# Optimization experiments

Hardware: AMD Instinct MI355X
Metric: run time of the kernel (lower is better)

## Reference

```python
import jax, jax.numpy as jnp
import numpy as np
from jax.ops import segment_sum

N0 = 50000
N1 = 50000
E = 300000
D = 128
L = 3
EPS_GIN = 0.1
COEF = 0.1
BN_EPS = 1e-5


def setup_inputs() -> dict:
    key = jax.random.key(0)
    ks = jax.random.split(key, 32)
    inp = {}
    inp['x0'] = jax.random.randint(ks[0], (N0, 2), 0, 3)
    inp['x1'] = jax.random.randint(ks[1], (N1, 2), 0, 3)
    inp['ei101'] = jax.random.randint(ks[2], (2, E), 0, N1)
    inp['ea101'] = jax.random.randint(ks[3], (E, 2), 0, 3)
    inp['ei110'] = jax.random.randint(ks[4], (2, E), 0, N0)  # src '1' -> dst '0' (N1==N0)
    inp['ea110'] = jax.random.randint(ks[5], (E, 2), 0, 3)
    inp['ei021'] = jax.random.randint(ks[6], (2, E), 0, N1)  # src '0' -> dst '1'
    inp['ea021'] = jax.random.randint(ks[7], (E, 2), 0, 3)
    inp['ei030'] = jax.random.randint(ks[8], (2, E), 0, N0)
    inp['ea030'] = jax.random.randint(ks[9], (E, 2), 0, 3)
    # learned parameters
    s = 0.05
    inp['x_emb1'] = jax.random.normal(ks[10], (120, D), jnp.float32) * s
    inp['x_emb2'] = jax.random.normal(ks[11], (3, D), jnp.float32) * s
    inp['e_emb1'] = jax.random.normal(ks[12], (6, D), jnp.float32) * s
    inp['e_emb2'] = jax.random.normal(ks[13], (3, D), jnp.float32) * s
    w = 1.0 / np.sqrt(D)
    inp['gin_w1'] = jax.random.normal(ks[14], (D, 2 * D), jnp.float32) * w
    inp['gin_b1'] = jnp.zeros((2 * D,), jnp.float32)
    inp['gin_w2'] = jax.random.normal(ks[15], (2 * D, D), jnp.float32) * (1.0 / np.sqrt(2 * D))
    inp['gin_b2'] = jnp.zeros((D,), jnp.float32)
    inp['w110'] = jax.random.normal(ks[16], (D, D), jnp.float32) * w
    inp['b110'] = jnp.zeros((D,), jnp.float32)
    inp['w021'] = jax.random.normal(ks[17], (D, D), jnp.float32) * w
    inp['b021'] = jnp.zeros((D,), jnp.float32)
    inp['w030'] = jax.random.normal(ks[18], (D, D), jnp.float32) * w
    inp['b030'] = jnp.zeros((D,), jnp.float32)
    inp['bn_gamma'] = jnp.ones((L, D), jnp.float32)
    inp['bn_beta'] = jnp.zeros((L, D), jnp.float32)
    return inp


def _add_self_loops(ei, ea, n):
    loop = jnp.arange(n, dtype=ei.dtype)
    ei = jnp.concatenate([ei, jnp.stack([loop, loop])], axis=1)
    self_attr = jnp.tile(jnp.array([[4, 0]], dtype=ea.dtype), (n, 1))
    return ei, jnp.concatenate([ea, self_attr], axis=0)


def _bn(x, gamma, beta):
    # training-mode BatchNorm1d: batch statistics, biased variance
    mu = jnp.mean(x, axis=0)
    var = jnp.var(x, axis=0)
    return (x - mu) * jax.lax.rsqrt(var + BN_EPS) * gamma + beta


def reference(x0, x1, ei101, ea101, ei110, ea110, ei021, ea021, ei030, ea030,
              x_emb1, x_emb2, e_emb1, e_emb2,
              gin_w1, gin_b1, gin_w2, gin_b2,
              w110, b110, w021, b021, w030, b030,
              bn_gamma, bn_beta):
    n0, n1 = x0.shape[0], x1.shape[0]
    # AddSelfLoops only for homogeneous edge types, fill_value=[4,0]
    ei101, ea101 = _add_self_loops(ei101, ea101, n1)
    ei030, ea030 = _add_self_loops(ei030, ea030, n0)

    h0 = x_emb1[x0[:, 0]] + x_emb2[x0[:, 1]]
    h1 = x_emb1[x1[:, 0]] + x_emb2[x1[:, 1]]
    e101 = e_emb1[ea101[:, 0]] + e_emb2[ea101[:, 1]]
    e110 = e_emb1[ea110[:, 0]] + e_emb2[ea110[:, 1]]
    e021 = e_emb1[ea021[:, 0]] + e_emb2[ea021[:, 1]]
    e030 = e_emb1[ea030[:, 0]] + e_emb2[ea030[:, 1]]

    def gin(h_src, h_dst, ei, eattr):
        agg = segment_sum(h_src[ei[0]] + eattr, ei[1], num_segments=h_dst.shape[0])
        z = agg + (1.0 + EPS_GIN) * h_dst
        return jnp.maximum(z @ gin_w1 + gin_b1, 0.0) @ gin_w2 + gin_b2

    def lin(h_src, n_dst, ei, eattr, w, b):
        agg = segment_sum(h_src[ei[0]] + eattr, ei[1], num_segments=n_dst)
        return (agg @ w + b) * COEF

    for layer in range(L):
        # HeteroConv aggr='mean' over convs sharing a destination node type
        out1 = 0.5 * (gin(h1, h1, ei101, e101) + lin(h0, n1, ei021, e021, w021, b021))
        out0 = 0.5 * (lin(h1, n0, ei110, e110, w110, b110) + lin(h0, n0, ei030, e030, w030, b030))
        g, b = bn_gamma[layer], bn_beta[layer]
        h0, h1 = _bn(out0, g, b), _bn(out1, g, b)
        if layer < L - 1:
            h0, h1 = jax.nn.relu(h0), jax.nn.relu(h1)
    # to_homogeneous().x: node types in order '0', '1'
    return jnp.concatenate([h0, h1], axis=0)
```

## Files before the change

### kernel.cpp

```cpp
#include <hip/hip_runtime.h>

#define D 128
#define BN_EPS 1e-5f
#define MAXNB 16

typedef __attribute__((ext_vector_type(8))) short bf16x8;
typedef __attribute__((ext_vector_type(4))) float f32x4;

__device__ __forceinline__ unsigned short f2bf(float x) {
  unsigned u = __float_as_uint(x);
  u += 0x7FFF + ((u >> 16) & 1);
  return (unsigned short)(u >> 16);
}

__device__ __forceinline__ void cvt8(float (&f)[8], bf16x8 r) {
  const unsigned* u = (const unsigned*)&r;
#pragma unroll
  for (int j = 0; j < 4; ++j) {
    f[2 * j] = __uint_as_float(u[j] << 16);
    f[2 * j + 1] = __uint_as_float(u[j] & 0xFFFF0000u);
  }
}

__global__ __launch_bounds__(256) void k_etbl(const float* __restrict__ e1,
                                              const float* __restrict__ e2,
                                              float* __restrict__ etbl) {
  int idx = blockIdx.x * 256 + threadIdx.x;
  if (idx < 9 * D) {
    int combo = idx / D, c = idx % D;
    etbl[idx] = e1[(combo / 3) * D + c] + e2[(combo % 3) * D + c];
  } else if (idx < 10 * D) {
    int c = idx - 9 * D;
    etbl[idx] = e1[4 * D + c] + e2[c];
  }
}

__global__ __launch_bounds__(256) void k_embed(const int* __restrict__ x,
                                               const float* __restrict__ emb1,
                                               const float* __restrict__ emb2,
                                               unsigned short* __restrict__ out,
                                               int n) {
  int idx = blockIdx.x * 256 + threadIdx.x;
  if (idx >= n * 32) return;
  int node = idx >> 5, c4 = idx & 31;
  int i1 = x[2 * node], i2 = x[2 * node + 1];
  float4 v1 = *(const float4*)(emb1 + (size_t)i1 * D + c4 * 4);
  float4 v2 = *(const float4*)(emb2 + (size_t)i2 * D + c4 * 4);
  ushort4 o;
  o.x = f2bf(v1.x + v2.x); o.y = f2bf(v1.y + v2.y);
  o.z = f2bf(v1.z + v2.z); o.w = f2bf(v1.w + v2.w);
  *(ushort4*)(out + (size_t)node * D + c4 * 4) = o;
}

__global__ __launch_bounds__(256) void k_wprep(const float* __restrict__ W,
                                               unsigned short* __restrict__ Wt,
                                               int K, int N, float scale) {
  int idx = blockIdx.x * 256 + threadIdx.x;
  if (idx >= K * N) return;
  int n = idx / K, k = idx - n * K;
  Wt[idx] = f2bf(W[(size_t)k * N + n] * scale);
}

__global__ __launch_bounds__(256) void k_bprep(
    const float* __restrict__ b110, const float* __restrict__ b030,
    const float* __restrict__ gb1, const float* __restrict__ gb2,
    const float* __restrict__ b021, float* __restrict__ bias0,
    float* __restrict__ biash, float* __restrict__ bias1) {
  int i = threadIdx.x;
  if (i < 128) {
    bias0[i] = 0.05f * (b110[i] + b030[i]);
    bias1[i] = 0.5f * gb2[i] + 0.05f * b021[i];
  }
  biash[i] = gb1[i];
}

#define ECHUNK 2048
struct EdgeArr {
  const int* ei[4];
  const int* ea[4];
  int* cur[4];
  int* pay[4];
};
struct CsrPtrs {
  int* cur[4];
  int* rp[4];
  int n[4];
};

__global__ __launch_bounds__(256) void k_hist_part(EdgeArr A, int E, int rsz) {
  int t = blockIdx.y;
  int r = blockIdx.x & 7;
  int chunk = blockIdx.x >> 3;
  const int* dstp = A.ei[t] + E;
  int* cur = A.cur[t];
  int lo = r * rsz, hi = lo + rsz;
  int base = chunk * ECHUNK;
  int end = min(base + ECHUNK, E);
  for (int e = base + (int)threadIdx.x; e < end; e += 256) {
    int dst = dstp[e];
    if (dst >= lo && dst < hi) atomicAdd(&cur[dst], 1);
  }
}

__global__ __launch_bounds__(256) void k_scan1(CsrPtrs p, int* __restrict__ bsum) {
  __shared__ int lds[256];
  int type = blockIdx.y;
  const int* cur = p.cur[type];
  int n = p.n[type];
  int base = blockIdx.x * 4096;
  int s = 0;
  for (int i = threadIdx.x; i < 4096; i += 256) {
    int idx = base + i;
    if (idx < n) s += cur[idx];
  }
  int tid = threadIdx.x;
  lds[tid] = s;
  __syncthreads();
  for (int off = 128; off > 0; off >>= 1) {
    if (tid < off) lds[tid] += lds[tid + off];
    __syncthreads();
  }
  if (tid == 0) bsum[type * MAXNB + blockIdx.x] = lds[0];
}

__global__ __launch_bounds__(64) void k_scan2(int* __restrict__ bsum) {
  int t = threadIdx.x;
  if (t < 4) {
    int run = 0;
    for (int i = 0; i < MAXNB; ++i) {
      int v = bsum[t * MAXNB + i];
      bsum[t * MAXNB + i] = run;
      run += v;
    }
  }
}

__global__ __launch_bounds__(256) void k_scan3(CsrPtrs p,
                                               const int* __restrict__ bsum,
                                               int E) {
  __shared__ int lds[256];
  int type = blockIdx.y;
  int* cur = p.cur[type];
  int* rp = p.rp[type];
  int n = p.n[type];
  int tid = threadIdx.x;
  if (blockIdx.x == 0 && tid == 0) rp[n] = E;
  int t0 = blockIdx.x * 4096 + tid * 16;
  int loc[16];
  int s = 0;
#pragma unroll
  for (int j = 0; j < 16; ++j) {
    int idx = t0 + j;
    int v = (idx < n) ? cur[idx] : 0;
    loc[j] = s;
    s += v;
  }
  lds[tid] = s;
  __syncthreads();
  for (int off = 1; off < 256; off <<= 1) {
    int v = (tid >= off) ? lds[tid - off] : 0;
    __syncthreads();
    lds[tid] += v;
    __syncthreads();
  }
  int off0 = bsum[type * MAXNB + blockIdx.x] + ((tid == 0) ? 0 : lds[tid - 1]);
#pragma unroll
  for (int j = 0; j < 16; ++j) {
    int idx = t0 + j;
    if (idx < n) {
      int v = off0 + loc[j];
      rp[idx] = v;
      cur[idx] = v;
    }
  }
}

__global__ __launch_bounds__(256) void k_fill_part(EdgeArr A, int E, int rsz) {
  int t = blockIdx.y;
  int r = blockIdx.x & 7;
  int chunk = blockIdx.x >> 3;
  const int* ei = A.ei[t];
  const int* ea = A.ea[t];
  int* cur = A.cur[t];
  int* pay = A.pay[t];
  int lo = r * rsz, hi = lo + rsz;
  int base = chunk * ECHUNK;
  int end = min(base + ECHUNK, E);
  for (int e = base + (int)threadIdx.x; e < end; e += 256) {
    int dst = ei[E + e];
    if (dst >= lo && dst < hi) {
      int src = ei[e];
      int combo = ea[2 * e] * 3 + ea[2 * e + 1];
      int pos = atomicAdd(&cur[dst], 1);
      pay[pos] = src | (combo << 16);
    }
  }
}

struct GArgs {
  const unsigned short* src[4];
  const unsigned short* base[4];
  const int* rp[4];
  const int* pay[4];
  unsigned short* agg[4];
  int mode[4];
  int n[4];
};

__global__ __launch_bounds__(256) void k_base(GArgs G,
                                              const float* __restrict__ etbl) {
  __shared__ float et[10 * D];
  for (int i = threadIdx.x; i < 10 * D; i += 256) et[i] = etbl[i];
  __syncthreads();
  int t = blockIdx.y;
  int n = G.n[t];
  int wv = threadIdx.x >> 6;
  int l = threadIdx.x & 63;
  int grp = l >> 4, sl = l & 15, c = sl * 8;
  const int* __restrict__ pay = G.pay[t];
  const int* __restrict__ rp = G.rp[t];
  unsigned short* __restrict__ outb = (unsigned short*)G.base[t];
  int mode = G.mode[t];
  int gbase = (blockIdx.x * 4 + wv) * 4;

  for (int i = 0; i < 4; ++i) {
    int g = gbase + i;
    if (g >= n) break;
    float acc[8];
    if (grp == 0 && mode != 0) {
#pragma unroll
      for (int j = 0; j < 8; ++j) acc[j] = et[9 * D + c + j];
    } else {
#pragma unroll
      for (int j = 0; j < 8; ++j) acc[j] = 0.f;
    }
    int e1 = rp[g + 1];
    for (int e = rp[g] + grp; e < e1; e += 4) {
      int combo = pay[e] >> 16;
      const float* etp = et + combo * D + c;
#pragma unroll
      for (int j = 0; j < 8; ++j) acc[j] += etp[j];
    }
#pragma unroll
    for (int j = 0; j < 8; ++j) {
      acc[j] += __shfl_xor(acc[j], 16);
      acc[j] += __shfl_xor(acc[j], 32);
    }
    if (grp == 0) {
      unsigned o0 = (unsigned)f2bf(acc[0]) | ((unsigned)f2bf(acc[1]) << 16);
      unsigned o1 = (unsigned)f2bf(acc[2]) | ((unsigned)f2bf(acc[3]) << 16);
      unsigned o2 = (unsigned)f2bf(acc[4]) | ((unsigned)f2bf(acc[5]) << 16);
      unsigned o3 = (unsigned)f2bf(acc[6]) | ((unsigned)f2bf(acc[7]) << 16);
      *(uint4*)(outb + (size_t)g * D + c) = make_uint4(o0, o1, o2, o3);
    }
  }
}

__global__ __launch_bounds__(256) void k_gather_all(GArgs G) {
  int t = blockIdx.y;
  int n = G.n[t];
  int wv = threadIdx.x >> 6;
  int l = threadIdx.x & 63;
  int grp = l >> 4, sl = l & 15, c = sl * 8;
  const unsigned short* __restrict__ hsrc = G.src[t];
  const unsigned short* __restrict__ baseb = G.base[t];
  const int* __restrict__ pay = G.pay[t];
  const int* __restrict__ rp = G.rp[t];
  unsigned short* __restrict__ agg = G.agg[t];
  int mode = G.mode[t];
  int gbase = (blockIdx.x * 4 + wv) * 4;

  for (int i = 0; i < 4; ++i) {
    int g = gbase + i;
    if (g >= n) break;
    float acc[8];
    if (grp == 0) {
      bf16x8 bv = *(const bf16x8*)(baseb + (size_t)g * D + c);
      cvt8(acc, bv);
      if (mode != 0) {
        bf16x8 hv = *(const bf16x8*)(hsrc + (size_t)g * D + c);
        float f[8];
        cvt8(f, hv);
        float m = (mode == 2) ? 2.1f : 1.0f;
#pragma unroll
        for (int j = 0; j < 8; ++j) acc[j] += m * f[j];
      }
    } else {
#pragma unroll
      for (int j = 0; j < 8; ++j) acc[j] = 0.f;
    }
    int e1 = rp[g + 1];
    int e = rp[g] + grp;
    while (e + 4 < e1) {
      int p0 = pay[e] & 0xFFFF;
      int p1 = pay[e + 4] & 0xFFFF;
      bf16x8 r0 = *(const bf16x8*)(hsrc + (size_t)p0 * D + c);
      bf16x8 r1 = *(const bf16x8*)(hsrc + (size_t)p1 * D + c);
      float f0[8], f1[8];
      cvt8(f0, r0);
      cvt8(f1, r1);
#pragma unroll
      for (int j = 0; j < 8; ++j) acc[j] += f0[j] + f1[j];
      e += 8;
    }
    if (e < e1) {
      int p0 = pay[e] & 0xFFFF;
      bf16x8 r0 = *(const bf16x8*)(hsrc + (size_t)p0 * D + c);
      float f0[8];
      cvt8(f0, r0);
#pragma unroll
      for (int j = 0; j < 8; ++j) acc[j] += f0[j];
    }
#pragma unroll
    for (int j = 0; j < 8; ++j) {
      acc[j] += __shfl_xor(acc[j], 16);
      acc[j] += __shfl_xor(acc[j], 32);
    }
    if (grp == 0) {
      unsigned o0 = (unsigned)f2bf(acc[0]) | ((unsigned)f2bf(acc[1]) << 16);
      unsigned o1 = (unsigned)f2bf(acc[2]) | ((unsigned)f2bf(acc[3]) << 16);
      unsigned o2 = (unsigned)f2bf(acc[4]) | ((unsigned)f2bf(acc[5]) << 16);
      unsigned o3 = (unsigned)f2bf(acc[6]) | ((unsigned)f2bf(acc[7]) << 16);
      *(uint4*)(agg + (size_t)g * D + c) = make_uint4(o0, o1, o2, o3);
    }
  }
}

__global__ __launch_bounds__(256) void k_hnorm(const unsigned short* __restrict__ h,
                                               unsigned short* __restrict__ hn,
                                               const float* __restrict__ bnp,
                                               int n) {
  int idx = blockIdx.x * 256 + threadIdx.x;
  if (idx >= n * 16) return;
  int node = idx >> 4, sl = idx & 15, c = sl * 8;
  bf16x8 v = *(const bf16x8*)(h + (size_t)node * D + c);
  float f[8];
  cvt8(f, v);
  unsigned o[4];
#pragma unroll
  for (int j = 0; j < 4; ++j) {
    float a = fmaxf(fmaf(f[2 * j], bnp[c + 2 * j], bnp[D + c + 2 * j]), 0.f);
    float b = fmaxf(fmaf(f[2 * j + 1], bnp[c + 2 * j + 1], bnp[D + c + 2 * j + 1]), 0.f);
    o[j] = (unsigned)f2bf(a) | ((unsigned)f2bf(b) << 16);
  }
  *(uint4*)(hn + (size_t)node * D + c) = make_uint4(o[0], o[1], o[2], o[3]);
}

template <int NCOLS, int K1, int K2, bool RELU, bool STATS, bool OBF16>
__global__ __launch_bounds__(256) void gemm_breg(
    const unsigned short* __restrict__ A1, const unsigned short* __restrict__ Wt1,
    const unsigned short* __restrict__ A2, const unsigned short* __restrict__ Wt2,
    const float* __restrict__ bias, void* __restrict__ Cv, int M,
    float* __restrict__ stats) {
  constexpr int WC = NCOLS / 4;
  constexpr int CF = WC / 16;
  constexpr int KF1 = K1 / 32;
  constexpr int KF2 = (K2 > 0) ? (K2 / 32) : 1;

  int tid = threadIdx.x;
  int w = tid >> 6, l = tid & 63;
  int lr = l & 15, lk = l >> 4;
  int colbase = w * WC;
  int row0 = blockIdx.x * 64;

  f32x4 acc[4][CF];
#pragma unroll
  for (int rf = 0; rf < 4; ++rf)
#pragma unroll
    for (int cf = 0; cf < CF; ++cf) acc[rf][cf] = (f32x4)(0.f);

  {
    const unsigned short* ap[4];
#pragma unroll
    for (int rf = 0; rf < 4; ++rf) {
      int r = row0 + rf * 16 + lr;
      if (r > M - 1) r = M - 1;
      ap[rf] = A1 + (size_t)r * K1 + lk * 8;
    }
    bf16x8 B[CF][KF1];
#pragma unroll
    for (int cf = 0; cf < CF; ++cf)
#pragma unroll
      for (int kf = 0; kf < KF1; ++kf)
        B[cf][kf] = *(const bf16x8*)(Wt1 + (size_t)(colbase + cf * 16 + lr) * K1 +
                                     kf * 32 + lk * 8);
#pragma unroll
    for (int kf = 0; kf < KF1; ++kf) {
      bf16x8 a[4];
#pragma unroll
      for (int rf = 0; rf < 4; ++rf) a[rf] = *(const bf16x8*)(ap[rf] + kf * 32);
#pragma unroll
      for (int rf = 0; rf < 4; ++rf)
#pragma unroll
        for (int cf = 0; cf < CF; ++cf)
          acc[rf][cf] = __builtin_amdgcn_mfma_f32_16x16x32_bf16(a[rf], B[cf][kf],
                                                                acc[rf][cf], 0, 0, 0);
    }
  }
  if constexpr (K2 > 0) {
    const unsigned short* ap[4];
#pragma unroll
    for (int rf = 0; rf < 4; ++rf) {
      int r = row0 + rf * 16 + lr;
      if (r > M - 1) r = M - 1;
      ap[rf] = A2 + (size_t)r * K2 + lk * 8;
    }
    bf16x8 B[CF][KF2];
#pragma unroll
    for (int cf = 0; cf < CF; ++cf)
#pragma unroll
      for (int kf = 0; kf < KF2; ++kf)
        B[cf][kf] = *(const bf16x8*)(Wt2 + (size_t)(colbase + cf * 16 + lr) * K2 +
                                     kf * 32 + lk * 8);
#pragma unroll
    for (int kf = 0; kf < KF2; ++kf) {
      bf16x8 a[4];
#pragma unroll
      for (int rf = 0; rf < 4; ++rf) a[rf] = *(const bf16x8*)(ap[rf] + kf * 32);
#pragma unroll
      for (int rf = 0; rf < 4; ++rf)
#pragma unroll
        for (int cf = 0; cf < CF; ++cf)
          acc[rf][cf] = __builtin_amdgcn_mfma_f32_16x16x32_bf16(a[rf], B[cf][kf],
                                                                acc[rf][cf], 0, 0, 0);
    }
  }

  float bv[CF];
#pragma unroll
  for (int cf = 0; cf < CF; ++cf) bv[cf] = bias[colbase + cf * 16 + lr];

  float colS[CF], colQ[CF];
#pragma unroll
  for (int cf = 0; cf < CF; ++cf) { colS[cf] = 0.f; colQ[cf] = 0.f; }

  float* Cf = (float*)Cv;
  unsigned short* Cb = (unsigned short*)Cv;
#pragma unroll
  for (int rf = 0; rf < 4; ++rf) {
#pragma unroll
    for (int r = 0; r < 4; ++r) {
      int row = row0 + rf * 16 + lk * 4 + r;
      bool ok = row < M;
#pragma unroll
      for (int cf = 0; cf < CF; ++cf) {
        int col = colbase + cf * 16 + lr;
        float v = acc[rf][cf][r] + bv[cf];
        if (RELU) v = fmaxf(v, 0.f);
        if (ok) {
          if (OBF16)
            Cb[(size_t)row * NCOLS + col] = f2bf(v);
          else
            Cf[(size_t)row * NCOLS + col] = v;
          if (STATS) { colS[cf] += v; colQ[cf] += v * v; }
        }
      }
    }
  }

  if constexpr (STATS) {
#pragma unroll
    for (int cf = 0; cf < CF; ++cf) {
      float s = colS[cf], q = colQ[cf];
      s += __shfl_xor(s, 16); q += __shfl_xor(q, 16);
      s += __shfl_xor(s, 32); q += __shfl_xor(q, 32);
      if (lk == 0) {
        int col = colbase + cf * 16 + lr;
        atomicAdd(&stats[col], s);
        atomicAdd(&stats[D + col], q);
      }
    }
  }
}

__global__ __launch_bounds__(256) void k_bnprep(const float* __restrict__ stats,
                                                const float* __restrict__ gamma,
                                                const float* __restrict__ beta,
                                                float* __restrict__ bnp0,
                                                float* __restrict__ bnp1,
                                                float invM0, float invM1) {
  int i = threadIdx.x;
  if (i < 128) {
    float mu = stats[i] * invM0;
    float var = stats[D + i] * invM0 - mu * mu;
    float sc = rsqrtf(var + BN_EPS) * gamma[i];
    bnp0[i] = sc;
    bnp0[D + i] = beta[i] - mu * sc;
  } else {
    int d = i - 128;
    float mu = stats[2 * D + d] * invM1;
    float var = stats[3 * D + d] * invM1 - mu * mu;
    float sc = rsqrtf(var + BN_EPS) * gamma[d];
    bnp1[d] = sc;
    bnp1[D + d] = beta[d] - mu * sc;
  }
}

__global__ __launch_bounds__(256) void k_bnfin(float* __restrict__ X, int M,
                                               const float* __restrict__ bnp) {
  int idx = blockIdx.x * 256 + threadIdx.x;
  int i = idx >> 5, c4 = idx & 31;
  if (i >= M) return;
  float4 v = *(float4*)(X + (size_t)i * D + c4 * 4);
  float4 sc = *(const float4*)(bnp + c4 * 4);
  float4 sh = *(const float4*)(bnp + D + c4 * 4);
  float4 o;
  o.x = fmaf(v.x, sc.x, sh.x); o.y = fmaf(v.y, sc.y, sh.y);
  o.z = fmaf(v.z, sc.z, sh.z); o.w = fmaf(v.w, sc.w, sh.w);
  *(float4*)(X + (size_t)i * D + c4 * 4) = o;
}

extern "C" void kernel_launch(void* const* d_in, const int* in_sizes, int n_in,
                              void* d_out, int out_size, void* d_ws,
                              size_t ws_size, hipStream_t stream) {
  const int* x0 = (const int*)d_in[0];
  const int* x1 = (const int*)d_in[1];
  const int* ei101 = (const int*)d_in[2];
  const int* ea101 = (const int*)d_in[3];
  const int* ei110 = (const int*)d_in[4];
  const int* ea110 = (const int*)d_in[5];
  const int* ei021 = (const int*)d_in[6];
  const int* ea021 = (const int*)d_in[7];
  const int* ei030 = (const int*)d_in[8];
  const int* ea030 = (const int*)d_in[9];
  const float* x_emb1 = (const float*)d_in[10];
  const float* x_emb2 = (const float*)d_in[11];
  const float* e_emb1 = (const float*)d_in[12];
  const float* e_emb2 = (const float*)d_in[13];
  const float* gin_w1 = (const float*)d_in[14];
  const float* gin_b1 = (const float*)d_in[15];
  const float* gin_w2 = (const float*)d_in[16];
  const float* gin_b2 = (const float*)d_in[17];
  const float* w110 = (const float*)d_in[18];
  const float* b110 = (const float*)d_in[19];
  const float* w021 = (const float*)d_in[20];
  const float* b021 = (const float*)d_in[21];
  const float* w030 = (const float*)d_in[22];
  const float* b030 = (const float*)d_in[23];
  const float* bn_gamma = (const float*)d_in[24];
  const float* bn_beta = (const float*)d_in[25];

  int n0 = in_sizes[0] / 2, n1 = in_sizes[1] / 2;
  int E = in_sizes[2] / 2;
  int nmax = n0 > n1 ? n0 : n1;

  float* h0f = (float*)d_out;
  float* h1f = h0f + (size_t)n0 * D;

  char* p = (char*)d_ws;
  auto alloc = [&](size_t bytes) {
    char* r = p;
    p += (bytes + 63) & ~(size_t)63;
    return r;
  };
  unsigned short* h0r = (unsigned short*)alloc((size_t)n0 * D * 2);
  unsigned short* h1r = (unsigned short*)alloc((size_t)n1 * D * 2);
  unsigned short* hn0 = (unsigned short*)alloc((size_t)n0 * D * 2);
  unsigned short* hn1 = (unsigned short*)alloc((size_t)n1 * D * 2);
  unsigned short* z1b = (unsigned short*)alloc((size_t)n1 * D * 2);
  unsigned short* a021b = (unsigned short*)alloc((size_t)n1 * D * 2);
  unsigned short* a110b = (unsigned short*)alloc((size_t)n0 * D * 2);
  unsigned short* a030b = (unsigned short*)alloc((size_t)n0 * D * 2);
  unsigned short* hiddenb = (unsigned short*)alloc((size_t)n1 * 256 * 2);
  unsigned short* baseb[4];
  for (int t = 0; t < 4; ++t)
    baseb[t] = (unsigned short*)alloc((size_t)nmax * D * 2);
  float* etbl = (float*)alloc(10 * D * 4);
  float* stats = (float*)alloc(4 * D * 4);
  float* bnp0 = (float*)alloc(2 * D * 4);
  float* bnp1 = (float*)alloc(2 * D * 4);
  unsigned short* wt110 = (unsigned short*)alloc(128 * 128 * 2);
  unsigned short* wt030 = (unsigned short*)alloc(128 * 128 * 2);
  unsigned short* wt021 = (unsigned short*)alloc(128 * 128 * 2);
  unsigned short* wtg1 = (unsigned short*)alloc(256 * 128 * 2);
  unsigned short* wtg2 = (unsigned short*)alloc(128 * 256 * 2);
  float* bias0 = (float*)alloc(128 * 4);
  float* biash = (float*)alloc(256 * 4);
  float* bias1 = (float*)alloc(128 * 4);

  EdgeArr EA;
  CsrPtrs cp;
  const int* eis[4] = {ei101, ei021, ei110, ei030};
  const int* eas[4] = {ea101, ea021, ea110, ea030};
  int ndst[4] = {n1, n1, n0, n0};
  for (int t = 0; t < 4; ++t) {
    cp.rp[t] = (int*)alloc((size_t)(nmax + 1) * 4);
    cp.cur[t] = (int*)alloc((size_t)nmax * 4);
    EA.pay[t] = (int*)alloc((size_t)E * 4);
    cp.n[t] = ndst[t];
    EA.ei[t] = eis[t];
    EA.ea[t] = eas[t];
    EA.cur[t] = cp.cur[t];
  }
  int* bsum = (int*)alloc(4 * MAXNB * 4);

  dim3 b256(256);

  k_etbl<<<5, b256, 0, stream>>>(e_emb1, e_emb2, etbl);
  k_embed<<<(n0 * 32 + 255) / 256, b256, 0, stream>>>(x0, x_emb1, x_emb2, h0r, n0);
  k_embed<<<(n1 * 32 + 255) / 256, b256, 0, stream>>>(x1, x_emb1, x_emb2, h1r, n1);
  k_wprep<<<64, b256, 0, stream>>>(w110, wt110, 128, 128, 0.05f);
  k_wprep<<<64, b256, 0, stream>>>(w030, wt030, 128, 128, 0.05f);
  k_wprep<<<64, b256, 0, stream>>>(w021, wt021, 128, 128, 0.05f);
  k_wprep<<<128, b256, 0, stream>>>(gin_w1, wtg1, 128, 256, 1.0f);
  k_wprep<<<128, b256, 0, stream>>>(gin_w2, wtg2, 256, 128, 0.5f);
  k_bprep<<<1, b256, 0, stream>>>(b110, b030, gin_b1, gin_b2, b021, bias0, biash, bias1);

  for (int t = 0; t < 4; ++t)
    hipMemsetAsync(cp.cur[t], 0, (size_t)ndst[t] * sizeof(int), stream);
  int rsz = (nmax + 7) / 8;
  int nchunks = (E + ECHUNK - 1) / ECHUNK;
  dim3 partGrid(nchunks * 8, 4);
  k_hist_part<<<partGrid, b256, 0, stream>>>(EA, E, rsz);
  hipMemsetAsync(bsum, 0, 4 * MAXNB * sizeof(int), stream);
  int nb = (nmax + 4095) / 4096;
  k_scan1<<<dim3(nb, 4), b256, 0, stream>>>(cp, bsum);
  k_scan2<<<1, dim3(64), 0, stream>>>(bsum);
  k_scan3<<<dim3(nb, 4), b256, 0, stream>>>(cp, bsum, E);
  k_fill_part<<<partGrid, b256, 0, stream>>>(EA, E, rsz);

  GArgs GA;
  GA.agg[0] = z1b;   GA.mode[0] = 2; GA.n[0] = n1;
  GA.agg[1] = a021b; GA.mode[1] = 0; GA.n[1] = n1;
  GA.agg[2] = a110b; GA.mode[2] = 0; GA.n[2] = n0;
  GA.agg[3] = a030b; GA.mode[3] = 1; GA.n[3] = n0;
  for (int t = 0; t < 4; ++t) {
    GA.rp[t] = cp.rp[t];
    GA.pay[t] = EA.pay[t];
    GA.base[t] = baseb[t];
  }

  dim3 gGrid((nmax + 15) / 16, 4);
  k_base<<<gGrid, b256, 0, stream>>>(GA, etbl);

  int mB0 = (n0 + 63) / 64, mB1 = (n1 + 63) / 64;

  for (int layer = 0; layer < 3; ++layer) {
    const unsigned short* s0 = (layer == 0) ? h0r : hn0;
    const unsigned short* s1 = (layer == 0) ? h1r : hn1;
    GA.src[0] = s1; GA.src[1] = s0; GA.src[2] = s1; GA.src[3] = s0;
    k_gather_all<<<gGrid, b256, 0, stream>>>(GA);

    hipMemsetAsync(stats, 0, 4 * D * sizeof(float), stream);

    if (layer < 2) {
      gemm_breg<128, 128, 128, false, true, true><<<mB0, b256, 0, stream>>>(
          a110b, wt110, a030b, wt030, bias0, h0r, n0, stats);
      gemm_breg<256, 128, 0, true, false, true><<<mB1, b256, 0, stream>>>(
          z1b, wtg1, nullptr, nullptr, biash, hiddenb, n1, nullptr);
      gemm_breg<128, 256, 128, false, true, true><<<mB1, b256, 0, stream>>>(
          hiddenb, wtg2, a021b, wt021, bias1, h1r, n1, stats + 2 * D);
    } else {
      gemm_breg<128, 128, 128, false, true, false><<<mB0, b256, 0, stream>>>(
          a110b, wt110, a030b, wt030, bias0, h0f, n0, stats);
      gemm_breg<256, 128, 0, true, false, true><<<mB1, b256, 0, stream>>>(
          z1b, wtg1, nullptr, nullptr, biash, hiddenb, n1, nullptr);
      gemm_breg<128, 256, 128, false, true, false><<<mB1, b256, 0, stream>>>(
          hiddenb, wtg2, a021b, wt021, bias1, h1f, n1, stats + 2 * D);
    }

    k_bnprep<<<1, b256, 0, stream>>>(stats, bn_gamma + layer * D,
                                     bn_beta + layer * D, bnp0, bnp1,
                                     1.0f / n0, 1.0f / n1);
    if (layer < 2) {
      k_hnorm<<<(n0 * 16 + 255) / 256, b256, 0, stream>>>(h0r, hn0, bnp0, n0);
      k_hnorm<<<(n1 * 16 + 255) / 256, b256, 0, stream>>>(h1r, hn1, bnp1, n1);
    } else {
      k_bnfin<<<(n0 * 32 + 255) / 256, b256, 0, stream>>>(h0f, n0, bnp0);
      k_bnfin<<<(n1 * 32 + 255) / 256, b256, 0, stream>>>(h1f, n1, bnp1);
    }
  }
}
```

Measured before the change: 836.0 us.

## Fold edge-embedding sums into GEMM epilogue via per-node combo counts

Edge-attribute contributions are no longer materialized as per-node bf16 base arrays and re-read by every gather. Instead, per-node counts of the 9 attribute combos are computed once, the embedding table is pre-multiplied by each weight matrix, and the GEMM epilogue adds count·etw terms. The self-loop embedding is folded into the biases. Gathers now read only neighbor features, and the payload stores a pre-scaled row offset. This saves base-array traffic per layer, at the cost of extra epilogue FMAs and count loads, and it assumes src*128 fits in 24 bits.

Result: slower. 882.5 us (+5.6%).

```diff
diff --git a/kernel.cpp b/kernel.cpp
--- a/kernel.cpp
+++ b/kernel.cpp
@@ -72,6 +72,27 @@
     bias1[i] = 0.5f * gb2[i] + 0.05f * b021[i];
   }
   biash[i] = gb1[i];
+}
+
+__global__ __launch_bounds__(256) void k_etw(const float* __restrict__ etbl,
+                                             const float* __restrict__ W,
+                                             float* __restrict__ etw, int N,
+                                             float scale) {
+  int idx = blockIdx.x * 256 + threadIdx.x;
+  if (idx >= 10 * N) return;
+  int combo = idx / N, col = idx - combo * N;
+  float s = 0.f;
+  for (int k = 0; k < 128; ++k) s += etbl[combo * 128 + k] * W[(size_t)k * N + col];
+  etw[idx] = s * scale;
+}
+
+__global__ __launch_bounds__(256) void k_bfix(float* __restrict__ biash,
+                                              float* __restrict__ bias0,
+                                              const float* __restrict__ etwg1,
+                                              const float* __restrict__ etw030) {
+  int i = threadIdx.x;
+  biash[i] += etwg1[9 * 256 + i];
+  if (i < 128) bias0[i] += etw030[9 * 128 + i];
 }
 
 #define ECHUNK 2048
@@ -192,138 +213,35 @@
       int src = ei[e];
       int combo = ea[2 * e] * 3 + ea[2 * e + 1];
       int pos = atomicAdd(&cur[dst], 1);
-      pay[pos] = src | (combo << 16);
-    }
-  }
-}
-
-struct GArgs {
-  const unsigned short* src[4];
-  const unsigned short* base[4];
+      pay[pos] = (combo << 24) | (src << 7);
+    }
+  }
+}
+
+struct CntArgs {
   const int* rp[4];
   const int* pay[4];
-  unsigned short* agg[4];
-  int mode[4];
+  float* cnt[4];
   int n[4];
 };
-
-__global__ __launch_bounds__(256) void k_base(GArgs G,
-                                              const float* __restrict__ etbl) {
-  __shared__ float et[10 * D];
-  for (int i = threadIdx.x; i < 10 * D; i += 256) et[i] = etbl[i];
-  __syncthreads();
+__global__ __launch_bounds__(256) void k_cnt(CntArgs A) {
   int t = blockIdx.y;
-  int n = G.n[t];
-  int wv = threadIdx.x >> 6;
-  int l = threadIdx.x & 63;
-  int grp = l >> 4, sl = l & 15, c = sl * 8;
-  const int* __restrict__ pay = G.pay[t];
-  const int* __restrict__ rp = G.rp[t];
-  unsigned short* __restrict__ outb = (unsigned short*)G.base[t];
-  int mode = G.mode[t];
-  int gbase = (blockIdx.x * 4 + wv) * 4;
-
-  for (int i = 0; i < 4; ++i) {
-    int g = gbase + i;
-    if (g >= n) break;
-    float acc[8];
-    if (grp == 0 && mode != 0) {
-#pragma unroll
-      for (int j = 0; j < 8; ++j) acc[j] = et[9 * D + c + j];
-    } else {
-#pragma unroll
-      for (int j = 0; j < 8; ++j) acc[j] = 0.f;
-    }
-    int e1 = rp[g + 1];
-    for (int e = rp[g] + grp; e < e1; e += 4) {
-      int combo = pay[e] >> 16;
-      const float* etp = et + combo * D + c;
-#pragma unroll
-      for (int j = 0; j < 8; ++j) acc[j] += etp[j];
-    }
-#pragma unroll
-    for (int j = 0; j < 8; ++j) {
-      acc[j] += __shfl_xor(acc[j], 16);
-      acc[j] += __shfl_xor(acc[j], 32);
-    }
-    if (grp == 0) {
-      unsigned o0 = (unsigned)f2bf(acc[0]) | ((unsigned)f2bf(acc[1]) << 16);
-      unsigned o1 = (unsigned)f2bf(acc[2]) | ((unsigned)f2bf(acc[3]) << 16);
-      unsigned o2 = (unsigned)f2bf(acc[4]) | ((unsigned)f2bf(acc[5]) << 16);
-      unsigned o3 = (unsigned)f2bf(acc[6]) | ((unsigned)f2bf(acc[7]) << 16);
-      *(uint4*)(outb + (size_t)g * D + c) = make_uint4(o0, o1, o2, o3);
-    }
-  }
-}
-
-__global__ __launch_bounds__(256) void k_gather_all(GArgs G) {
-  int t = blockIdx.y;
-  int n = G.n[t];
-  int wv = threadIdx.x >> 6;
-  int l = threadIdx.x & 63;
-  int grp = l >> 4, sl = l & 15, c = sl * 8;
-  const unsigned short* __restrict__ hsrc = G.src[t];
-  const unsigned short* __restrict__ baseb = G.base[t];
-  const int* __restrict__ pay = G.pay[t];
-  const int* __restrict__ rp = G.rp[t];
-  unsigned short* __restrict__ agg = G.agg[t];
-  int mode = G.mode[t];
-  int gbase = (blockIdx.x * 4 + wv) * 4;
-
-  for (int i = 0; i < 4; ++i) {
-    int g = gbase + i;
-    if (g >= n) break;
-    float acc[8];
-    if (grp == 0) {
-      bf16x8 bv = *(const bf16x8*)(baseb + (size_t)g * D + c);
-      cvt8(acc, bv);
-      if (mode != 0) {
-        bf16x8 hv = *(const bf16x8*)(hsrc + (size_t)g * D + c);
-        float f[8];
-        cvt8(f, hv);
-        float m = (mode == 2) ? 2.1f : 1.0f;
-#pragma unroll
-        for (int j = 0; j < 8; ++j) acc[j] += m * f[j];
-      }
-    } else {
-#pragma unroll
-      for (int j = 0; j < 8; ++j) acc[j] = 0.f;
-    }
-    int e1 = rp[g + 1];
-    int e = rp[g] + grp;
-    while (e + 4 < e1) {
-      int p0 = pay[e] & 0xFFFF;
-      int p1 = pay[e + 4] & 0xFFFF;
-      bf16x8 r0 = *(const bf16x8*)(hsrc + (size_t)p0 * D + c);
-      bf16x8 r1 = *(const bf16x8*)(hsrc + (size_t)p1 * D + c);
-      float f0[8], f1[8];
-      cvt8(f0, r0);
-      cvt8(f1, r1);
-#pragma unroll
-      for (int j = 0; j < 8; ++j) acc[j] += f0[j] + f1[j];
-      e += 8;
-    }
-    if (e < e1) {
-      int p0 = pay[e] & 0xFFFF;
-      bf16x8 r0 = *(const bf16x8*)(hsrc + (size_t)p0 * D + c);
-      float f0[8];
-      cvt8(f0, r0);
-#pragma unroll
-      for (int j = 0; j < 8; ++j) acc[j] += f0[j];
-    }
-#pragma unroll
-    for (int j = 0; j < 8; ++j) {
-      acc[j] += __shfl_xor(acc[j], 16);
-      acc[j] += __shfl_xor(acc[j], 32);
-    }
-    if (grp == 0) {
-      unsigned o0 = (unsigned)f2bf(acc[0]) | ((unsigned)f2bf(acc[1]) << 16);
-      unsigned o1 = (unsigned)f2bf(acc[2]) | ((unsigned)f2bf(acc[3]) << 16);
-      unsigned o2 = (unsigned)f2bf(acc[4]) | ((unsigned)f2bf(acc[5]) << 16);
-      unsigned o3 = (unsigned)f2bf(acc[6]) | ((unsigned)f2bf(acc[7]) << 16);
-      *(uint4*)(agg + (size_t)g * D + c) = make_uint4(o0, o1, o2, o3);
-    }
-  }
+  int g = blockIdx.x * 256 + threadIdx.x;
+  if (g >= A.n[t]) return;
+  const int* pay = A.pay[t];
+  int e0 = A.rp[t][g], e1 = A.rp[t][g + 1];
+  float cc[9];
+#pragma unroll
+  for (int j = 0; j < 9; ++j) cc[j] = 0.f;
+  for (int e = e0; e < e1; ++e) {
+    int cb = pay[e] >> 24;
+#pragma unroll
+    for (int j = 0; j < 9; ++j) cc[j] += (cb == j) ? 1.f : 0.f;
+  }
+  float* o = A.cnt[t] + (size_t)g * 12;
+  *(float4*)(o) = make_float4(cc[0], cc[1], cc[2], cc[3]);
+  *(float4*)(o + 4) = make_float4(cc[4], cc[5], cc[6], cc[7]);
+  *(float4*)(o + 8) = make_float4(cc[8], 0.f, 0.f, 0.f);
 }
 
 __global__ __launch_bounds__(256) void k_hnorm(const unsigned short* __restrict__ h,
@@ -346,12 +264,89 @@
   *(uint4*)(hn + (size_t)node * D + c) = make_uint4(o[0], o[1], o[2], o[3]);
 }
 
-template <int NCOLS, int K1, int K2, bool RELU, bool STATS, bool OBF16>
+struct GArgs {
+  const unsigned short* src[4];
+  const int* rp[4];
+  const int* pay[4];
+  unsigned short* agg[4];
+  int mode[4];
+  int n[4];
+};
+
+__global__ __launch_bounds__(256) void k_gather_all(GArgs G) {
+  int t = blockIdx.y;
+  int n = G.n[t];
+  int wv = threadIdx.x >> 6;
+  int l = threadIdx.x & 63;
+  int grp = l >> 4, sl = l & 15, c = sl * 8;
+  const unsigned short* __restrict__ hsrc = G.src[t];
+  const int* __restrict__ pay = G.pay[t];
+  const int* __restrict__ rp = G.rp[t];
+  unsigned short* __restrict__ agg = G.agg[t];
+  int mode = G.mode[t];
+  int gbase = (blockIdx.x * 4 + wv) * 4;
+
+  for (int i = 0; i < 4; ++i) {
+    int g = gbase + i;
+    if (g >= n) break;
+    float acc[8];
+    if (grp == 0 && mode != 0) {
+      bf16x8 hv = *(const bf16x8*)(hsrc + (size_t)g * D + c);
+      float f[8];
+      cvt8(f, hv);
+      float m = (mode == 2) ? 2.1f : 1.0f;
+#pragma unroll
+      for (int j = 0; j < 8; ++j) acc[j] = m * f[j];
+    } else {
+#pragma unroll
+      for (int j = 0; j < 8; ++j) acc[j] = 0.f;
+    }
+    int e1 = rp[g + 1];
+    int e = rp[g] + grp;
+    while (e + 4 < e1) {
+      int p0 = pay[e] & 0xFFFFFF;
+      int p1 = pay[e + 4] & 0xFFFFFF;
+      bf16x8 r0 = *(const bf16x8*)(hsrc + (size_t)p0 + c);
+      bf16x8 r1 = *(const bf16x8*)(hsrc + (size_t)p1 + c);
+      float f0[8], f1[8];
+      cvt8(f0, r0);
+      cvt8(f1, r1);
+#pragma unroll
+      for (int j = 0; j < 8; ++j) acc[j] += f0[j] + f1[j];
+      e += 8;
+    }
+    if (e < e1) {
+      int p0 = pay[e] & 0xFFFFFF;
+      bf16x8 r0 = *(const bf16x8*)(hsrc + (size_t)p0 + c);
+      float f0[8];
+      cvt8(f0, r0);
+#pragma unroll
+      for (int j = 0; j < 8; ++j) acc[j] += f0[j];
+    }
+#pragma unroll
+    for (int j = 0; j < 8; ++j) {
+      acc[j] += __shfl_xor(acc[j], 16);
+      acc[j] += __shfl_xor(acc[j], 32);
+    }
+    if (grp == 0) {
+      unsigned o0 = (unsigned)f2bf(acc[0]) | ((unsigned)f2bf(acc[1]) << 16);
+      unsigned o1 = (unsigned)f2bf(acc[2]) | ((unsigned)f2bf(acc[3]) << 16);
+      unsigned o2 = (unsigned)f2bf(acc[4]) | ((unsigned)f2bf(acc[5]) << 16);
+      unsigned o3 = (unsigned)f2bf(acc[6]) | ((unsigned)f2bf(acc[7]) << 16);
+      *(uint4*)(agg + (size_t)g * D + c) = make_uint4(o0, o1, o2, o3);
+    }
+  }
+}
+
+template <int NCOLS, int K1, int K2, bool RELU, bool STATS, bool OBF16,
+          bool C1, bool C2>
 __global__ __launch_bounds__(256) void gemm_breg(
     const unsigned short* __restrict__ A1, const unsigned short* __restrict__ Wt1,
     const unsigned short* __restrict__ A2, const unsigned short* __restrict__ Wt2,
     const float* __restrict__ bias, void* __restrict__ Cv, int M,
-    float* __restrict__ stats) {
+    float* __restrict__ stats, const float* __restrict__ cnt1,
+    const float* __restrict__ etw1, const float* __restrict__ cnt2,
+    const float* __restrict__ etw2) {
   constexpr int WC = NCOLS / 4;
   constexpr int CF = WC / 16;
   constexpr int KF1 = K1 / 32;
@@ -430,6 +425,22 @@
 #pragma unroll
   for (int cf = 0; cf < CF; ++cf) bv[cf] = bias[colbase + cf * 16 + lr];
 
+  float ew1[C1 ? CF : 1][9], ew2[C2 ? CF : 1][9];
+  if constexpr (C1) {
+#pragma unroll
+    for (int cf = 0; cf < CF; ++cf)
+#pragma unroll
+      for (int cb = 0; cb < 9; ++cb)
+        ew1[cf][cb] = etw1[cb * NCOLS + colbase + cf * 16 + lr];
+  }
+  if constexpr (C2) {
+#pragma unroll
+    for (int cf = 0; cf < CF; ++cf)
+#pragma unroll
+      for (int cb = 0; cb < 9; ++cb)
+        ew2[cf][cb] = etw2[cb * NCOLS + colbase + cf * 16 + lr];
+  }
+
   float colS[CF], colQ[CF];
 #pragma unroll
   for (int cf = 0; cf < CF; ++cf) { colS[cf] = 0.f; colQ[cf] = 0.f; }
@@ -442,10 +453,36 @@
     for (int r = 0; r < 4; ++r) {
       int row = row0 + rf * 16 + lk * 4 + r;
       bool ok = row < M;
+      int crow = ok ? row : 0;
+      float cv1[9], cv2[9];
+      if constexpr (C1) {
+        float4 a = *(const float4*)(cnt1 + (size_t)crow * 12);
+        float4 b = *(const float4*)(cnt1 + (size_t)crow * 12 + 4);
+        float4 cc = *(const float4*)(cnt1 + (size_t)crow * 12 + 8);
+        cv1[0] = a.x; cv1[1] = a.y; cv1[2] = a.z; cv1[3] = a.w;
+        cv1[4] = b.x; cv1[5] = b.y; cv1[6] = b.z; cv1[7] = b.w;
+        cv1[8] = cc.x;
+      }
+      if constexpr (C2) {
+        float4 a = *(const float4*)(cnt2 + (size_t)crow * 12);
+        float4 b = *(const float4*)(cnt2 + (size_t)crow * 12 + 4);
+        float4 cc = *(const float4*)(cnt2 + (size_t)crow * 12 + 8);
+        cv2[0] = a.x; cv2[1] = a.y; cv2[2] = a.z; cv2[3] = a.w;
+        cv2[4] = b.x; cv2[5] = b.y; cv2[6] = b.z; cv2[7] = b.w;
+        cv2[8] = cc.x;
+      }
 #pragma unroll
       for (int cf = 0; cf < CF; ++cf) {
         int col = colbase + cf * 16 + lr;
         float v = acc[rf][cf][r] + bv[cf];
+        if constexpr (C1) {
+#pragma unroll
+          for (int cb = 0; cb < 9; ++cb) v = fmaf(cv1[cb], ew1[cf][cb], v);
+        }
+        if constexpr (C2) {
+#pragma unroll
+          for (int cb = 0; cb < 9; ++cb) v = fmaf(cv2[cb], ew2[cf][cb], v);
+        }
         if (RELU) v = fmaxf(v, 0.f);
         if (ok) {
           if (OBF16)
@@ -562,9 +599,6 @@
   unsigned short* a110b = (unsigned short*)alloc((size_t)n0 * D * 2);
   unsigned short* a030b = (unsigned short*)alloc((size_t)n0 * D * 2);
   unsigned short* hiddenb = (unsigned short*)alloc((size_t)n1 * 256 * 2);
-  unsigned short* baseb[4];
-  for (int t = 0; t < 4; ++t)
-    baseb[t] = (unsigned short*)alloc((size_t)nmax * D * 2);
   float* etbl = (float*)alloc(10 * D * 4);
   float* stats = (float*)alloc(4 * D * 4);
   float* bnp0 = (float*)alloc(2 * D * 4);
@@ -577,9 +611,14 @@
   float* bias0 = (float*)alloc(128 * 4);
   float* biash = (float*)alloc(256 * 4);
   float* bias1 = (float*)alloc(128 * 4);
+  float* etwg1 = (float*)alloc(10 * 256 * 4);
+  float* etw021 = (float*)alloc(10 * 128 * 4);
+  float* etw110 = (float*)alloc(10 * 128 * 4);
+  float* etw030 = (float*)alloc(10 * 128 * 4);
 
   EdgeArr EA;
   CsrPtrs cp;
+  CntArgs CA;
   const int* eis[4] = {ei101, ei021, ei110, ei030};
   const int* eas[4] = {ea101, ea021, ea110, ea030};
   int ndst[4] = {n1, n1, n0, n0};
@@ -587,10 +626,14 @@
     cp.rp[t] = (int*)alloc((size_t)(nmax + 1) * 4);
     cp.cur[t] = (int*)alloc((size_t)nmax * 4);
     EA.pay[t] = (int*)alloc((size_t)E * 4);
+    CA.cnt[t] = (float*)alloc((size_t)nmax * 12 * 4);
     cp.n[t] = ndst[t];
     EA.ei[t] = eis[t];
     EA.ea[t] = eas[t];
     EA.cur[t] = cp.cur[t];
+    CA.rp[t] = cp.rp[t];
+    CA.pay[t] = EA.pay[t];
+    CA.n[t] = ndst[t];
   }
   int* bsum = (int*)alloc(4 * MAXNB * 4);
 
@@ -605,6 +648,11 @@
   k_wprep<<<128, b256, 0, stream>>>(gin_w1, wtg1, 128, 256, 1.0f);
   k_wprep<<<128, b256, 0, stream>>>(gin_w2, wtg2, 256, 128, 0.5f);
   k_bprep<<<1, b256, 0, stream>>>(b110, b030, gin_b1, gin_b2, b021, bias0, biash, bias1);
+  k_etw<<<10, b256, 0, stream>>>(etbl, gin_w1, etwg1, 256, 1.0f);
+  k_etw<<<5, b256, 0, stream>>>(etbl, w021, etw021, 128, 0.05f);
+  k_etw<<<5, b256, 0, stream>>>(etbl, w110, etw110, 128, 0.05f);
+  k_etw<<<5, b256, 0, stream>>>(etbl, w030, etw030, 128, 0.05f);
+  k_bfix<<<1, b256, 0, stream>>>(biash, bias0, etwg1, etw030);
 
   for (int t = 0; t < 4; ++t)
     hipMemsetAsync(cp.cur[t], 0, (size_t)ndst[t] * sizeof(int), stream);
@@ -618,6 +666,7 @@
   k_scan2<<<1, dim3(64), 0, stream>>>(bsum);
   k_scan3<<<dim3(nb, 4), b256, 0, stream>>>(cp, bsum, E);
   k_fill_part<<<partGrid, b256, 0, stream>>>(EA, E, rsz);
+  k_cnt<<<dim3((nmax + 255) / 256, 4), b256, 0, stream>>>(CA);
 
   GArgs GA;
   GA.agg[0] = z1b;   GA.mode[0] = 2; GA.n[0] = n1;
@@ -627,13 +676,10 @@
   for (int t = 0; t < 4; ++t) {
     GA.rp[t] = cp.rp[t];
     GA.pay[t] = EA.pay[t];
-    GA.base[t] = baseb[t];
-  }
-
+  }
+
+  int mB0 = (n0 + 63) / 64, mB1 = (n1 + 63) / 64;
   dim3 gGrid((nmax + 15) / 16, 4);
-  k_base<<<gGrid, b256, 0, stream>>>(GA, etbl);
-
-  int mB0 = (n0 + 63) / 64, mB1 = (n1 + 63) / 64;
 
   for (int layer = 0; layer < 3; ++layer) {
     const unsigned short* s0 = (layer == 0) ? h0r : hn0;
@@ -644,19 +690,25 @@
     hipMemsetAsync(stats, 0, 4 * D * sizeof(float), stream);
 
     if (layer < 2) {
-      gemm_breg<128, 128, 128, false, true, true><<<mB0, b256, 0, stream>>>(
-          a110b, wt110, a030b, wt030, bias0, h0r, n0, stats);
-      gemm_breg<256, 128, 0, true, false, true><<<mB1, b256, 0, stream>>>(
-          z1b, wtg1, nullptr, nullptr, biash, hiddenb, n1, nullptr);
-      gemm_breg<128, 256, 128, false, true, true><<<mB1, b256, 0, stream>>>(
-          hiddenb, wtg2, a021b, wt021, bias1, h1r, n1, stats + 2 * D);
+      gemm_breg<128, 128, 128, false, true, true, true, true>
+          <<<mB0, b256, 0, stream>>>(a110b, wt110, a030b, wt030, bias0, h0r, n0,
+                                     stats, CA.cnt[2], etw110, CA.cnt[3], etw030);
+      gemm_breg<256, 128, 0, true, false, true, true, false>
+          <<<mB1, b256, 0, stream>>>(z1b, wtg1, nullptr, nullptr, biash, hiddenb,
+                                     n1, nullptr, CA.cnt[0], etwg1, nullptr, nullptr);
+      gemm_breg<128, 256, 128, false, true, true, false, true>
+          <<<mB1, b256, 0, stream>>>(hiddenb, wtg2, a021b, wt021, bias1, h1r, n1,
+                                     stats + 2 * D, nullptr, nullptr, CA.cnt[1], etw021);
     } else {
-      gemm_breg<128, 128, 128, false, true, false><<<mB0, b256, 0, stream>>>(
-          a110b, wt110, a030b, wt030, bias0, h0f, n0, stats);
-      gemm_breg<256, 128, 0, true, false, true><<<mB1, b256, 0, stream>>>(
-          z1b, wtg1, nullptr, nullptr, biash, hiddenb, n1, nullptr);
-      gemm_breg<128, 256, 128, false, true, false><<<mB1, b256, 0, stream>>>(
-          hiddenb, wtg2, a021b, wt021, bias1, h1f, n1, stats + 2 * D);
+      gemm_breg<128, 128, 128, false, true, false, true, true>
+          <<<mB0, b256, 0, stream>>>(a110b, wt110, a030b, wt030, bias0, h0f, n0,
+                                     stats, CA.cnt[2], etw110, CA.cnt[3], etw030);
+      gemm_breg<256, 128, 0, true, false, true, true, false>
+          <<<mB1, b256, 0, stream>>>(z1b, wtg1, nullptr, nullptr, biash, hiddenb,
+                                     n1, nullptr, CA.cnt[0], etwg1, nullptr, nullptr);
+      gemm_breg<128, 256, 128, false, true, false, false, true>
+          <<<mB1, b256, 0, stream>>>(hiddenb, wtg2, a021b, wt021, bias1, h1f, n1,
+                                     stats + 2 * D, nullptr, nullptr, CA.cnt[1], etw021);
     }
 
     k_bnprep<<<1, b256, 0, stream>>>(stats, bn_gamma + layer * D,
```
